# Optimization experiments

Measured on AMD Instinct MI355X. Metric: run time of the kernel, lower is better.

The kernel has to match this reference:

```python
import jax, jax.numpy as jnp
import numpy as np

N, E, EMB, H, HD, T, NG = 2048, 65536, 256, 8, 32, 24, 8


def _linear_params(key, din, dout):
    k1, k2 = jax.random.split(key)
    s = 1.0 / np.sqrt(din)
    W = jax.random.uniform(k1, (din, dout), minval=-s, maxval=s, dtype=jnp.float32)
    b = jax.random.uniform(k2, (dout,), minval=-s, maxval=s, dtype=jnp.float32)
    return W, b


def setup_inputs() -> dict:
    key = jax.random.key(0)
    ks = jax.random.split(key, 16)
    x = jax.random.normal(ks[0], (N, EMB), dtype=jnp.float32)
    edge_index = jax.random.randint(ks[1], (2, E), 0, N, dtype=jnp.int64)
    edge_attr = jax.random.normal(ks[2], (E, 4), dtype=jnp.float32)
    batch = jnp.sort(jax.random.randint(ks[3], (N,), 0, NG, dtype=jnp.int64))
    time_index = jax.random.randint(ks[4], (N,), 0, T, dtype=jnp.int64)
    temporal_embeddings = jax.random.normal(ks[5], (T, EMB), dtype=jnp.float32)
    Wq, bq = _linear_params(ks[6], EMB, EMB)
    Wk, bk = _linear_params(ks[7], EMB, EMB)
    Wv, bv = _linear_params(ks[8], EMB, EMB)
    Wo, bo = _linear_params(ks[9], EMB, EMB)
    We, be = _linear_params(ks[10], 4, H)
    Wtq, btq = _linear_params(ks[11], EMB, EMB)
    Wtk, btk = _linear_params(ks[12], EMB, EMB)
    Wtv, btv = _linear_params(ks[13], EMB, EMB)
    return dict(x=x, edge_index=edge_index, edge_attr=edge_attr, batch=batch,
                time_index=time_index, temporal_embeddings=temporal_embeddings,
                Wq=Wq, bq=bq, Wk=Wk, bk=bk, Wv=Wv, bv=bv, Wo=Wo, bo=bo,
                We=We, be=be, Wtq=Wtq, btq=btq, Wtk=Wtk, btk=btk, Wtv=Wtv, btv=btv)


def _heads(X, n):
    # [n, EMB] -> [H, n, HD]
    return X.reshape(n, H, HD).transpose(1, 0, 2)


def reference(x, edge_index, edge_attr, batch, time_index, temporal_embeddings,
              Wq, bq, Wk, bk, Wv, bv, Wo, bo, We, be, Wtq, btq, Wtk, btk, Wtv, btv):
    n = x.shape[0]
    scale = HD ** -0.5

    Qh = _heads(x @ Wq + bq, n)
    Kh = _heads(x @ Wk + bk, n)
    Vh = _heads(x @ Wv + bv, n)
    scores = jnp.einsum('hnd,hmd->hnm', Qh, Kh) * scale  # [H, n, n]

    # edge bias: vectorized scatter-add of per-edge per-head biases into [H, n, n]
    src, dst = edge_index[0], edge_index[1]
    valid = (src >= 0) & (src < n) & (dst >= 0) & (dst < n)
    eb = edge_attr @ We + be                              # [E, H]
    eb = jnp.where(valid[:, None], eb, 0.0)
    srcc = jnp.clip(src, 0, n - 1)
    dstc = jnp.clip(dst, 0, n - 1)
    scores = scores.at[:, srcc, dstc].add(eb.T)

    # batch mask: nodes may only attend within their own graph
    same_graph = batch[:, None] == batch[None, :]          # [n, n]
    scores = jnp.where(same_graph[None, :, :], scores, -jnp.inf)

    attn = jax.nn.softmax(scores, axis=-1)
    spatial_out = jnp.einsum('hnm,hmd->hnd', attn, Vh)     # [H, n, HD]

    # temporal attention on gathered temporal embeddings
    ti = jnp.clip(time_index, 0, temporal_embeddings.shape[0] - 1)
    emb = temporal_embeddings[ti]                          # [n, EMB]
    TQ = _heads(emb @ Wtq + btq, n)
    TK = _heads(emb @ Wtk + btk, n)
    TV = _heads(emb @ Wtv + btv, n)
    t_scores = jnp.einsum('hnd,hmd->hnm', TQ, TK) * scale
    t_scores = jnp.where(same_graph[None, :, :], t_scores, -jnp.inf)
    t_attn = jax.nn.softmax(t_scores, axis=-1)
    temporal_out = jnp.einsum('hnm,hmd->hnd', t_attn, TV)

    combined = (spatial_out + temporal_out).transpose(1, 0, 2).reshape(n, EMB)
    return combined @ Wo + bo
```

## Files before the change

### kernel.cpp

```cpp
#include <hip/hip_runtime.h>
#include <cstdint>
#include <cstddef>

#define EMB 256
#define NH 8
#define HD 32
#define NG 8
#define TMAX 24

#define LMAX 384
#define LB 384
#define TPB 6
#define VRU 200
#define FM 8.0f

typedef short s16x8 __attribute__((ext_vector_type(8)));
typedef float f32x4 __attribute__((ext_vector_type(4)));

__device__ __forceinline__ unsigned short f2b(float f) {
    unsigned u = __float_as_uint(f);
    return (unsigned short)((u + 0x7FFFu + ((u >> 16) & 1u)) >> 16);
}
__device__ __forceinline__ float b2f(unsigned short h) {
    return __uint_as_float((unsigned)h << 16);
}
__device__ __forceinline__ unsigned long long pack4(unsigned short a, unsigned short b,
                                                    unsigned short c, unsigned short d) {
    return (unsigned long long)a | ((unsigned long long)b << 16) |
           ((unsigned long long)c << 32) | ((unsigned long long)d << 48);
}

__device__ __forceinline__ size_t afrag_idx(int row, int k) {
    return ((size_t)((row >> 4) * 8 + (k >> 5)) << 9) +
           ((((k >> 3) & 3) * 16 + (row & 15)) << 3) + (k & 7);
}

struct PrepArgs {
    float4* Bias4; int bias4;
    const float* x; unsigned short* xh; unsigned short* xl;
    const float* temb; const int* ti; unsigned short* eh; unsigned short* el;
    const float* W[7]; unsigned short* whb; unsigned short* wlb;
    const int* batch; int* gstart; int n;
    int zb, cvtb;
};

__global__ __launch_bounds__(256) void k_prep(PrepArgs pa) {
    __shared__ float tile[32][33];
    int b = blockIdx.x;
    const int t = threadIdx.x;

    if (b < pa.zb) {
        int i = b * 256 + t;
        if (i < pa.bias4) pa.Bias4[i] = make_float4(0.f, 0.f, 0.f, 0.f);
        return;
    }
    b -= pa.zb;
    if (b < pa.cvtb) {
        int i = b * 256 + t;
        if (i < pa.n * (EMB / 4)) {
            int row = i >> 6, k4 = (i & 63) * 4;
            float4 v = ((const float4*)pa.x)[i];
            unsigned short h0 = f2b(v.x), h1 = f2b(v.y), h2 = f2b(v.z), h3 = f2b(v.w);
            size_t o = afrag_idx(row, k4) >> 2;
            ((unsigned long long*)pa.xh)[o] = pack4(h0, h1, h2, h3);
            ((unsigned long long*)pa.xl)[o] = pack4(f2b(v.x - b2f(h0)), f2b(v.y - b2f(h1)),
                                                    f2b(v.z - b2f(h2)), f2b(v.w - b2f(h3)));
        }
        return;
    }
    b -= pa.cvtb;
    if (b < pa.cvtb) {
        int idx = b * 256 + t;
        if (idx < pa.n * (EMB / 4)) {
            int row = idx >> 6, k4 = (idx & 63) * 4;
            int tt = pa.ti[row];
            tt = tt < 0 ? 0 : (tt > TMAX - 1 ? TMAX - 1 : tt);
            float4 v = ((const float4*)pa.temb)[tt * (EMB / 4) + (idx & 63)];
            unsigned short h0 = f2b(v.x), h1 = f2b(v.y), h2 = f2b(v.z), h3 = f2b(v.w);
            size_t o = afrag_idx(row, k4) >> 2;
            ((unsigned long long*)pa.eh)[o] = pack4(h0, h1, h2, h3);
            ((unsigned long long*)pa.el)[o] = pack4(f2b(v.x - b2f(h0)), f2b(v.y - b2f(h1)),
                                                    f2b(v.z - b2f(h2)), f2b(v.w - b2f(h3)));
        }
        return;
    }
    b -= pa.cvtb;
    if (b < 448) {
        const int z = b >> 6, rem = b & 63;
        const int k0 = (rem >> 3) << 5, n0 = (rem & 7) << 5;
        const float* W = pa.W[z];
        unsigned short* Wh = pa.whb + (size_t)z * 65536;
        unsigned short* Wl = pa.wlb + (size_t)z * 65536;
        {
            int rr = t >> 3, c4 = (t & 7) * 4;
            float4 v = *(const float4*)(W + (size_t)(k0 + rr) * 256 + n0 + c4);
            tile[rr][c4 + 0] = v.x; tile[rr][c4 + 1] = v.y;
            tile[rr][c4 + 2] = v.z; tile[rr][c4 + 3] = v.w;
        }
        __syncthreads();
        {
            int nn = n0 + (t >> 3), k4 = (t & 7) * 4;
            float v0 = tile[k4 + 0][t >> 3], v1 = tile[k4 + 1][t >> 3];
            float v2 = tile[k4 + 2][t >> 3], v3 = tile[k4 + 3][t >> 3];
            unsigned short h0 = f2b(v0), h1 = f2b(v1), h2 = f2b(v2), h3 = f2b(v3);
            size_t o = afrag_idx(nn, k0 + k4) >> 2;
            ((unsigned long long*)Wh)[o] = pack4(h0, h1, h2, h3);
            ((unsigned long long*)Wl)[o] = pack4(f2b(v0 - b2f(h0)), f2b(v1 - b2f(h1)),
                                                 f2b(v2 - b2f(h2)), f2b(v3 - b2f(h3)));
        }
        return;
    }
    if (t <= NG) {
        int lo = 0, hi = pa.n;
        while (lo < hi) {
            int mid = (lo + hi) >> 1;
            if (pa.batch[mid] < t) lo = mid + 1; else hi = mid;
        }
        pa.gstart[t] = lo;
    }
}

struct GB {
    const unsigned short* Ah[6];
    const unsigned short* Al[6];
    const float* bias[6];
    unsigned short* Chi[6];
    unsigned short* Clo[6];
    float cscale[6];
};

__global__ __launch_bounds__(256) void k_gemm_split(GB gb,
        const unsigned short* __restrict__ whb, const unsigned short* __restrict__ wlb, int M,
        const int* __restrict__ ei, const float* __restrict__ eattr,
        const float* __restrict__ We, const float* __restrict__ be,
        const int* __restrict__ batch, const int* __restrict__ gstart,
        float* __restrict__ Bias, int E) {
    const int z = blockIdx.z;
    const int t = threadIdx.x;

    if (z == 6) {
        const int stride = gridDim.x * gridDim.y * 256;
        for (int e = (blockIdx.y * gridDim.x + blockIdx.x) * 256 + t; e < E; e += stride) {
            int src = ei[e], dst = ei[E + e];
            if (src < 0 || src >= M || dst < 0 || dst >= M) continue;
            int bs = batch[src];
            if (bs != batch[dst]) continue;
            float4 a = *(const float4*)(eattr + (size_t)e * 4);
            int col = dst - gstart[bs];
#pragma unroll
            for (int h = 0; h < NH; h++) {
                float v = a.x * We[0 * NH + h] + a.y * We[1 * NH + h] +
                          a.z * We[2 * NH + h] + a.w * We[3 * NH + h] + be[h];
                atomicAdd(Bias + ((size_t)h * M + src) * LB + col, v);
            }
        }
        return;
    }

    const unsigned short* Ah = gb.Ah[z];
    const unsigned short* Al = gb.Al[z];
    const unsigned short* Wh = whb + (size_t)z * 65536;
    const unsigned short* Wl = wlb + (size_t)z * 65536;
    const float* bias = gb.bias[z];
    unsigned short* Chi = gb.Chi[z];
    unsigned short* Clo = gb.Clo[z];
    const float cs = gb.cscale[z];
    const bool fs = (Clo != nullptr);

    const int lane = t & 63, wv = t >> 6, lr = lane & 15, lq = lane >> 4;
    const int bm = blockIdx.x * 64 + (wv >> 1) * 32;
    const int bn = blockIdx.y * 64 + (wv & 1) * 32;
    const int mg0 = bm >> 4, ng0 = bn >> 4;

    f32x4 acc[2][2] = {};
#pragma unroll
    for (int kc = 0; kc < 8; kc++) {
        s16x8 ah[2], al[2], bh[2], bl[2];
#pragma unroll
        for (int mi = 0; mi < 2; mi++) {
            size_t o = ((size_t)((mg0 + mi) * 8 + kc) << 9) + lane * 8;
            ah[mi] = *(const s16x8*)(Ah + o);
            if (fs) al[mi] = *(const s16x8*)(Al + o);
        }
#pragma unroll
        for (int ni = 0; ni < 2; ni++) {
            size_t o = ((size_t)((ng0 + ni) * 8 + kc) << 9) + lane * 8;
            bh[ni] = *(const s16x8*)(Wh + o);
            bl[ni] = *(const s16x8*)(Wl + o);
        }
#pragma unroll
        for (int mi = 0; mi < 2; mi++)
#pragma unroll
            for (int ni = 0; ni < 2; ni++) {
                if (fs)
                    acc[mi][ni] = __builtin_amdgcn_mfma_f32_16x16x32_bf16(al[mi], bh[ni], acc[mi][ni], 0, 0, 0);
                acc[mi][ni] = __builtin_amdgcn_mfma_f32_16x16x32_bf16(ah[mi], bl[ni], acc[mi][ni], 0, 0, 0);
                acc[mi][ni] = __builtin_amdgcn_mfma_f32_16x16x32_bf16(ah[mi], bh[ni], acc[mi][ni], 0, 0, 0);
            }
    }
#pragma unroll
    for (int ni = 0; ni < 2; ni++) {
        const int col = bn + ni * 16 + lr;
        const int hh = col >> 5, dd = col & 31;
        float bv = bias[col];
#pragma unroll
        for (int mi = 0; mi < 2; mi++) {
#pragma unroll
            for (int r = 0; r < 4; r++) {
                int crow = bm + mi * 16 + 4 * lq + r;
                if (crow < M) {
                    float val = (acc[mi][ni][r] + bv) * cs;
                    unsigned short h = f2b(val);
                    size_t o = ((size_t)hh * M + crow) * HD + dd;
                    Chi[o] = h;
                    if (fs) Clo[o] = f2b(val - b2f(h));
                }
            }
        }
    }
}

__global__ __launch_bounds__(256) void k_attn5(
    const unsigned short* __restrict__ Qh, const unsigned short* __restrict__ Ql,
    const unsigned short* __restrict__ K, const unsigned short* __restrict__ V,
    const unsigned short* __restrict__ TQh, const unsigned short* __restrict__ TQl,
    const unsigned short* __restrict__ TK, const unsigned short* __restrict__ TV,
    const int* __restrict__ gstart, const float* __restrict__ Bias,
    float* __restrict__ comb, int n) {

    const int g  = blockIdx.x / TPB;
    const int tp = blockIdx.x % TPB;
    const int h  = blockIdx.y;
    const int gs = gstart[g], ge = gstart[g + 1];
    const int L  = ge - gs;
    const int q0b = tp * 64;
    if (q0b >= L) return;
    const int NC = (L + 31) >> 5;

    __shared__ __align__(16) unsigned int Vt[32 * VRU];
    __shared__ __align__(16) unsigned short Pb[4][16][40];

    const int t = threadIdx.x;
    const int wv = t >> 6, lane = t & 63;
    const int lr = lane & 15, lq = lane >> 4;
    const size_t hb = (size_t)h * n;

    const int q0w = q0b + wv * 16;
    int gq = gs + q0w + lr;
    if (gq > ge - 1) gq = ge - 1;

    float os0[4] = {0.f, 0.f, 0.f, 0.f};
    float os1[4] = {0.f, 0.f, 0.f, 0.f};

    for (int tz = 0; tz < 2; tz++) {
        const unsigned short* Qph = tz ? TQh : Qh;
        const unsigned short* Qpl = tz ? TQl : Ql;
        const unsigned short* Kp  = tz ? TK  : K;
        const unsigned short* Vp  = tz ? TV  : V;
        const bool hasb = (tz == 0);

        if (tz) __syncthreads();

        {
            const int d0 = (t & 7) * 4;
            for (int jp = t >> 3; jp < NC * 16; jp += 32) {
                int j0 = jp * 2;
                unsigned short a0 = 0, a1 = 0, a2 = 0, a3 = 0, b0 = 0, b1 = 0, b2 = 0, b3 = 0;
                if (j0 < L) {
                    const unsigned short* vp = Vp + (hb + gs + j0) * HD + d0;
                    a0 = vp[0]; a1 = vp[1]; a2 = vp[2]; a3 = vp[3];
                }
                if (j0 + 1 < L) {
                    const unsigned short* vp = Vp + (hb + gs + j0 + 1) * HD + d0;
                    b0 = vp[0]; b1 = vp[1]; b2 = vp[2]; b3 = vp[3];
                }
                Vt[(d0 + 0) * VRU + jp] = (unsigned)a0 | ((unsigned)b0 << 16);
                Vt[(d0 + 1) * VRU + jp] = (unsigned)a1 | ((unsigned)b1 << 16);
                Vt[(d0 + 2) * VRU + jp] = (unsigned)a2 | ((unsigned)b2 << 16);
                Vt[(d0 + 3) * VRU + jp] = (unsigned)a3 | ((unsigned)b3 << 16);
            }
        }

        s16x8 qfh = *(const s16x8*)(Qph + (hb + gq) * HD + lq * 8);
        s16x8 qfl = *(const s16x8*)(Qpl + (hb + gq) * HD + lq * 8);
        __syncthreads();

        const float* br0 = Bias; const float* br1 = Bias;
        const float* br2 = Bias; const float* br3 = Bias;
        if (hasb) {
            int r0 = gs + q0w + 4 * lq;
            int a0 = r0 + 0 < n ? r0 + 0 : n - 1;
            int a1 = r0 + 1 < n ? r0 + 1 : n - 1;
            int a2 = r0 + 2 < n ? r0 + 2 : n - 1;
            int a3 = r0 + 3 < n ? r0 + 3 : n - 1;
            br0 = Bias + (hb + a0) * LB;
            br1 = Bias + (hb + a1) * LB;
            br2 = Bias + (hb + a2) * LB;
            br3 = Bias + (hb + a3) * LB;
        }

        auto loadK = [&](int c, int half) -> s16x8 {
            int key = (2 * c + half) * 16 + lr;
            int krow = (key < L) ? (gs + key) : (ge - 1);
            return *(const s16x8*)(Kp + (hb + krow) * HD + lq * 8);
        };

        f32x4 acc0 = {0.f, 0.f, 0.f, 0.f};
        f32x4 acc1 = {0.f, 0.f, 0.f, 0.f};
        float ps0 = 0.f, ps1 = 0.f, ps2 = 0.f, ps3 = 0.f;

        s16x8 kfa = loadK(0, 0), kfb = loadK(0, 1);
        for (int c = 0; c < NC; c++) {
            const int cn = (c + 1 < NC) ? c + 1 : c;
            s16x8 nka = loadK(cn, 0), nkb = loadK(cn, 1);

            float p[2][4];
#pragma unroll
            for (int half = 0; half < 2; half++) {
                const int key = (2 * c + half) * 16 + lr;
                s16x8 kf = half ? kfb : kfa;
                f32x4 d = {0.f, 0.f, 0.f, 0.f};
                d = __builtin_amdgcn_mfma_f32_16x16x32_bf16(qfl, kf, d, 0, 0, 0);
                d = __builtin_amdgcn_mfma_f32_16x16x32_bf16(qfh, kf, d, 0, 0, 0);
                float s0 = d[0], s1 = d[1], s2 = d[2], s3 = d[3];
                if (hasb) {
                    s0 += br0[key]; s1 += br1[key]; s2 += br2[key]; s3 += br3[key];
                }
                const bool ok = key < L;
                s0 = ok ? s0 : -3.0e38f;
                s1 = ok ? s1 : -3.0e38f;
                s2 = ok ? s2 : -3.0e38f;
                s3 = ok ? s3 : -3.0e38f;
                p[half][0] = __expf(s0 - FM);
                p[half][1] = __expf(s1 - FM);
                p[half][2] = __expf(s2 - FM);
                p[half][3] = __expf(s3 - FM);
            }
            ps0 += p[0][0] + p[1][0];
            ps1 += p[0][1] + p[1][1];
            ps2 += p[0][2] + p[1][2];
            ps3 += p[0][3] + p[1][3];
#pragma unroll
            for (int half = 0; half < 2; half++) {
#pragma unroll
                for (int r = 0; r < 4; r++)
                    Pb[wv][4 * lq + r][half * 16 + lr] = f2b(p[half][r]);
            }
            s16x8 pf  = *(const s16x8*)&Pb[wv][lr][8 * lq];
            s16x8 vf0 = *(const s16x8*)&Vt[(size_t)lr * VRU + c * 16 + lq * 4];
            s16x8 vf1 = *(const s16x8*)&Vt[(size_t)(16 + lr) * VRU + c * 16 + lq * 4];
            acc0 = __builtin_amdgcn_mfma_f32_16x16x32_bf16(pf, vf0, acc0, 0, 0, 0);
            acc1 = __builtin_amdgcn_mfma_f32_16x16x32_bf16(pf, vf1, acc1, 0, 0, 0);
            kfa = nka; kfb = nkb;
        }

#pragma unroll
        for (int m = 1; m < 16; m <<= 1) {
            ps0 += __shfl_xor(ps0, m, 16);
            ps1 += __shfl_xor(ps1, m, 16);
            ps2 += __shfl_xor(ps2, m, 16);
            ps3 += __shfl_xor(ps3, m, 16);
        }
        float iv0 = 1.0f / ps0, iv1 = 1.0f / ps1, iv2 = 1.0f / ps2, iv3 = 1.0f / ps3;
        os0[0] += acc0[0] * iv0; os1[0] += acc1[0] * iv0;
        os0[1] += acc0[1] * iv1; os1[1] += acc1[1] * iv1;
        os0[2] += acc0[2] * iv2; os1[2] += acc1[2] * iv2;
        os0[3] += acc0[3] * iv3; os1[3] += acc1[3] * iv3;
    }

    const int qb = q0w + 4 * lq;
#pragma unroll
    for (int r = 0; r < 4; r++) {
        if (qb + r < L) {
            float* op = comb + (hb + gs + qb + r) * HD + lr;
            op[0]  = os0[r];
            op[16] = os1[r];
        }
    }
}

__global__ __launch_bounds__(256) void k_gemm_out(const float* __restrict__ A,
        const unsigned short* __restrict__ Wh, const unsigned short* __restrict__ Wl,
        const float* __restrict__ bias, float* __restrict__ C, int M) {
    const int t = threadIdx.x;
    const int lane = t & 63, wv = t >> 6, lr = lane & 15, lq = lane >> 4;
    const int bm = blockIdx.x * 64 + (wv >> 1) * 32;
    const int bn = blockIdx.y * 64 + (wv & 1) * 32;
    const int ng0 = bn >> 4;

    int ra[2], cb[2];
#pragma unroll
    for (int mi = 0; mi < 2; mi++) {
        int r = bm + mi * 16 + lr;
        ra[mi] = r < M ? r : M - 1;
    }
#pragma unroll
    for (int ni = 0; ni < 2; ni++) cb[ni] = bn + ni * 16 + lr;

    f32x4 acc[2][2] = {};
#pragma unroll
    for (int kc = 0; kc < 8; kc++) {
        s16x8 ah[2], al[2], bh[2], bl[2];
#pragma unroll
        for (int mi = 0; mi < 2; mi++) {
            size_t off = ((size_t)kc * M + ra[mi]) * HD + lq * 8;
            float4 a = *(const float4*)(A + off);
            float4 b = *(const float4*)(A + off + 4);
            float vv[8] = {a.x, a.y, a.z, a.w, b.x, b.y, b.z, b.w};
#pragma unroll
            for (int j = 0; j < 8; j++) {
                unsigned short hh = f2b(vv[j]);
                ah[mi][j] = (short)hh;
                al[mi][j] = (short)f2b(vv[j] - b2f(hh));
            }
        }
#pragma unroll
        for (int ni = 0; ni < 2; ni++) {
            size_t o = ((size_t)((ng0 + ni) * 8 + kc) << 9) + lane * 8;
            bh[ni] = *(const s16x8*)(Wh + o);
            bl[ni] = *(const s16x8*)(Wl + o);
        }
#pragma unroll
        for (int mi = 0; mi < 2; mi++)
#pragma unroll
            for (int ni = 0; ni < 2; ni++) {
                acc[mi][ni] = __builtin_amdgcn_mfma_f32_16x16x32_bf16(al[mi], bh[ni], acc[mi][ni], 0, 0, 0);
                acc[mi][ni] = __builtin_amdgcn_mfma_f32_16x16x32_bf16(ah[mi], bl[ni], acc[mi][ni], 0, 0, 0);
                acc[mi][ni] = __builtin_amdgcn_mfma_f32_16x16x32_bf16(ah[mi], bh[ni], acc[mi][ni], 0, 0, 0);
            }
    }
#pragma unroll
    for (int ni = 0; ni < 2; ni++) {
        float bv = bias[cb[ni]];
#pragma unroll
        for (int mi = 0; mi < 2; mi++) {
#pragma unroll
            for (int r = 0; r < 4; r++) {
                int crow = bm + mi * 16 + 4 * lq + r;
                if (crow < M)
                    C[(size_t)crow * 256 + cb[ni]] = acc[mi][ni][r] + bv;
            }
        }
    }
}

extern "C" void kernel_launch(void* const* d_in, const int* in_sizes, int n_in,
                              void* d_out, int out_size, void* d_ws, size_t ws_size,
                              hipStream_t stream) {
    const float* x     = (const float*)d_in[0];
    const int*   ei    = (const int*)d_in[1];
    const float* eattr = (const float*)d_in[2];
    const int*   batch = (const int*)d_in[3];
    const int*   ti    = (const int*)d_in[4];
    const float* temb  = (const float*)d_in[5];
    const float* Wq = (const float*)d_in[6],  *bq = (const float*)d_in[7];
    const float* Wk = (const float*)d_in[8],  *bk = (const float*)d_in[9];
    const float* Wv = (const float*)d_in[10], *bv = (const float*)d_in[11];
    const float* Wo = (const float*)d_in[12], *bo = (const float*)d_in[13];
    const float* We = (const float*)d_in[14], *be = (const float*)d_in[15];
    const float* Wtq = (const float*)d_in[16], *btq = (const float*)d_in[17];
    const float* Wtk = (const float*)d_in[18], *btk = (const float*)d_in[19];
    const float* Wtv = (const float*)d_in[20], *btv = (const float*)d_in[21];

    const int n = in_sizes[0] / EMB;
    const int E = in_sizes[2] / 4;
    float* out = (float*)d_out;

    char* w = (char*)d_ws;
    auto alloc = [&](size_t bytes) -> void* {
        void* p = (void*)w;
        w += (bytes + 255) & ~(size_t)255;
        return p;
    };
    const size_t nb = (size_t)n * EMB * 2;
    unsigned short* xh   = (unsigned short*)alloc(nb);
    unsigned short* xl   = (unsigned short*)alloc(nb);
    unsigned short* eh   = (unsigned short*)alloc(nb);
    unsigned short* el   = (unsigned short*)alloc(nb);
    unsigned short* whb  = (unsigned short*)alloc((size_t)7 * 65536 * 2);
    unsigned short* wlb  = (unsigned short*)alloc((size_t)7 * 65536 * 2);
    unsigned short* Qhb  = (unsigned short*)alloc(nb);
    unsigned short* Qlb  = (unsigned short*)alloc(nb);
    unsigned short* Kb   = (unsigned short*)alloc(nb);
    unsigned short* Vb   = (unsigned short*)alloc(nb);
    unsigned short* TQhb = (unsigned short*)alloc(nb);
    unsigned short* TQlb = (unsigned short*)alloc(nb);
    unsigned short* TKb  = (unsigned short*)alloc(nb);
    unsigned short* TVb  = (unsigned short*)alloc(nb);
    float* Bias  = (float*)alloc((size_t)NH * n * LB * 4);
    float* comb  = (float*)alloc((size_t)n * EMB * 4);
    int* gstart  = (int*)alloc((NG + 1) * 4);

    PrepArgs pa;
    pa.Bias4 = (float4*)Bias;
    pa.bias4 = NH * n * LB / 4;
    pa.x = x; pa.xh = xh; pa.xl = xl;
    pa.temb = temb; pa.ti = ti; pa.eh = eh; pa.el = el;
    pa.W[0] = Wq; pa.W[1] = Wk; pa.W[2] = Wv;
    pa.W[3] = Wtq; pa.W[4] = Wtk; pa.W[5] = Wtv; pa.W[6] = Wo;
    pa.whb = whb; pa.wlb = wlb;
    pa.batch = batch; pa.gstart = gstart; pa.n = n;
    pa.zb = (pa.bias4 + 255) / 256;
    pa.cvtb = (n * (EMB / 4) + 255) / 256;
    const int prep_blocks = pa.zb + 2 * pa.cvtb + 448 + 1;
    k_prep<<<dim3(prep_blocks), dim3(256), 0, stream>>>(pa);

    const float scale = 0.17677669529663687f;
    GB gb;
    gb.Ah[0] = xh; gb.Al[0] = xl; gb.bias[0] = bq;  gb.Chi[0] = Qhb;  gb.Clo[0] = Qlb;  gb.cscale[0] = scale;
    gb.Ah[1] = xh; gb.Al[1] = xl; gb.bias[1] = bk;  gb.Chi[1] = Kb;   gb.Clo[1] = nullptr; gb.cscale[1] = 1.f;
    gb.Ah[2] = xh; gb.Al[2] = xl; gb.bias[2] = bv;  gb.Chi[2] = Vb;   gb.Clo[2] = nullptr; gb.cscale[2] = 1.f;
    gb.Ah[3] = eh; gb.Al[3] = el; gb.bias[3] = btq; gb.Chi[3] = TQhb; gb.Clo[3] = TQlb; gb.cscale[3] = scale;
    gb.Ah[4] = eh; gb.Al[4] = el; gb.bias[4] = btk; gb.Chi[4] = TKb;  gb.Clo[4] = nullptr; gb.cscale[4] = 1.f;
    gb.Ah[5] = eh; gb.Al[5] = el; gb.bias[5] = btv; gb.Chi[5] = TVb;  gb.Clo[5] = nullptr; gb.cscale[5] = 1.f;
    k_gemm_split<<<dim3((n + 63) / 64, EMB / 64, 7), dim3(256), 0, stream>>>(
        gb, whb, wlb, n, ei, eattr, We, be, batch, gstart, Bias, E);

    k_attn5<<<dim3(NG * TPB, NH), dim3(256), 0, stream>>>(Qhb, Qlb, Kb, Vb,
                                                          TQhb, TQlb, TKb, TVb,
                                                          gstart, Bias, comb, n);
    k_gemm_out<<<dim3((n + 63) / 64, EMB / 64), dim3(256), 0, stream>>>(
        comb, whb + (size_t)6 * 65536, wlb + (size_t)6 * 65536, bo, out, n);
}
```

Before: 61.01 us.

## Split attention key range across two blocks and merge partials in output GEMM

The attention kernel now splits each graph's key chunks across a new grid dimension of two, writing unnormalized partial P·V accumulators and row sums to scratch buffers. The output GEMM reads both partials for spatial and temporal attention, sums them, and normalizes before converting to bf16 hi/lo. Since a fixed max offset is used, no max rescaling is needed for the merge. This doubles the attention grid to improve occupancy on the many-CU device, in exchange for extra scratch writes and reads and more work in the output GEMM's load path.

```diff
diff --git a/kernel.cpp b/kernel.cpp
--- a/kernel.cpp
+++ b/kernel.cpp
@@ -13,6 +13,7 @@
 #define TPB 6
 #define VRU 200
 #define FM 8.0f
+#define KS 2
 
 typedef short s16x8 __attribute__((ext_vector_type(8)));
 typedef float f32x4 __attribute__((ext_vector_type(4)));
@@ -220,22 +221,26 @@
     }
 }
 
-__global__ __launch_bounds__(256) void k_attn5(
+__global__ __launch_bounds__(256) void k_attn6(
     const unsigned short* __restrict__ Qh, const unsigned short* __restrict__ Ql,
     const unsigned short* __restrict__ K, const unsigned short* __restrict__ V,
     const unsigned short* __restrict__ TQh, const unsigned short* __restrict__ TQl,
     const unsigned short* __restrict__ TK, const unsigned short* __restrict__ TV,
     const int* __restrict__ gstart, const float* __restrict__ Bias,
-    float* __restrict__ comb, int n) {
+    float* __restrict__ U, float* __restrict__ PS, int n) {
 
     const int g  = blockIdx.x / TPB;
     const int tp = blockIdx.x % TPB;
     const int h  = blockIdx.y;
+    const int ks = blockIdx.z;
     const int gs = gstart[g], ge = gstart[g + 1];
     const int L  = ge - gs;
     const int q0b = tp * 64;
     if (q0b >= L) return;
-    const int NC = (L + 31) >> 5;
+    const int NC  = (L + 31) >> 5;
+    const int NCH = (NC + KS - 1) / KS;
+    const int c0  = ks * NCH;
+    const int c1  = (c0 + NCH < NC) ? (c0 + NCH) : NC;
 
     __shared__ __align__(16) unsigned int Vt[32 * VRU];
     __shared__ __align__(16) unsigned short Pb[4][16][40];
@@ -248,9 +253,7 @@
     const int q0w = q0b + wv * 16;
     int gq = gs + q0w + lr;
     if (gq > ge - 1) gq = ge - 1;
-
-    float os0[4] = {0.f, 0.f, 0.f, 0.f};
-    float os1[4] = {0.f, 0.f, 0.f, 0.f};
+    const int qb = q0w + 4 * lq;
 
     for (int tz = 0; tz < 2; tz++) {
         const unsigned short* Qph = tz ? TQh : Qh;
@@ -262,9 +265,10 @@
         if (tz) __syncthreads();
 
         {
+            const int NPAIR = (c1 - c0) * 16;
             const int d0 = (t & 7) * 4;
-            for (int jp = t >> 3; jp < NC * 16; jp += 32) {
-                int j0 = jp * 2;
+            for (int jp = t >> 3; jp < NPAIR; jp += 32) {
+                int j0 = c0 * 32 + jp * 2;
                 unsigned short a0 = 0, a1 = 0, a2 = 0, a3 = 0, b0 = 0, b1 = 0, b2 = 0, b3 = 0;
                 if (j0 < L) {
                     const unsigned short* vp = Vp + (hb + gs + j0) * HD + d0;
@@ -309,49 +313,51 @@
         f32x4 acc1 = {0.f, 0.f, 0.f, 0.f};
         float ps0 = 0.f, ps1 = 0.f, ps2 = 0.f, ps3 = 0.f;
 
-        s16x8 kfa = loadK(0, 0), kfb = loadK(0, 1);
-        for (int c = 0; c < NC; c++) {
-            const int cn = (c + 1 < NC) ? c + 1 : c;
-            s16x8 nka = loadK(cn, 0), nkb = loadK(cn, 1);
-
-            float p[2][4];
-#pragma unroll
-            for (int half = 0; half < 2; half++) {
-                const int key = (2 * c + half) * 16 + lr;
-                s16x8 kf = half ? kfb : kfa;
-                f32x4 d = {0.f, 0.f, 0.f, 0.f};
-                d = __builtin_amdgcn_mfma_f32_16x16x32_bf16(qfl, kf, d, 0, 0, 0);
-                d = __builtin_amdgcn_mfma_f32_16x16x32_bf16(qfh, kf, d, 0, 0, 0);
-                float s0 = d[0], s1 = d[1], s2 = d[2], s3 = d[3];
-                if (hasb) {
-                    s0 += br0[key]; s1 += br1[key]; s2 += br2[key]; s3 += br3[key];
+        if (c0 < c1) {
+            s16x8 kfa = loadK(c0, 0), kfb = loadK(c0, 1);
+            for (int c = c0; c < c1; c++) {
+                const int cn = (c + 1 < c1) ? c + 1 : c;
+                s16x8 nka = loadK(cn, 0), nkb = loadK(cn, 1);
+
+                float p[2][4];
+#pragma unroll
+                for (int half = 0; half < 2; half++) {
+                    const int key = (2 * c + half) * 16 + lr;
+                    s16x8 kf = half ? kfb : kfa;
+                    f32x4 d = {0.f, 0.f, 0.f, 0.f};
+                    d = __builtin_amdgcn_mfma_f32_16x16x32_bf16(qfl, kf, d, 0, 0, 0);
+                    d = __builtin_amdgcn_mfma_f32_16x16x32_bf16(qfh, kf, d, 0, 0, 0);
+                    float s0 = d[0], s1 = d[1], s2 = d[2], s3 = d[3];
+                    if (hasb) {
+                        s0 += br0[key]; s1 += br1[key]; s2 += br2[key]; s3 += br3[key];
+                    }
+                    const bool ok = key < L;
+                    s0 = ok ? s0 : -3.0e38f;
+                    s1 = ok ? s1 : -3.0e38f;
+                    s2 = ok ? s2 : -3.0e38f;
+                    s3 = ok ? s3 : -3.0e38f;
+                    p[half][0] = __expf(s0 - FM);
+                    p[half][1] = __expf(s1 - FM);
+                    p[half][2] = __expf(s2 - FM);
+                    p[half][3] = __expf(s3 - FM);
                 }
-                const bool ok = key < L;
-                s0 = ok ? s0 : -3.0e38f;
-                s1 = ok ? s1 : -3.0e38f;
-                s2 = ok ? s2 : -3.0e38f;
-                s3 = ok ? s3 : -3.0e38f;
-                p[half][0] = __expf(s0 - FM);
-                p[half][1] = __expf(s1 - FM);
-                p[half][2] = __expf(s2 - FM);
-                p[half][3] = __expf(s3 - FM);
-            }
-            ps0 += p[0][0] + p[1][0];
-            ps1 += p[0][1] + p[1][1];
-            ps2 += p[0][2] + p[1][2];
-            ps3 += p[0][3] + p[1][3];
-#pragma unroll
-            for (int half = 0; half < 2; half++) {
-#pragma unroll
-                for (int r = 0; r < 4; r++)
-                    Pb[wv][4 * lq + r][half * 16 + lr] = f2b(p[half][r]);
-            }
-            s16x8 pf  = *(const s16x8*)&Pb[wv][lr][8 * lq];
-            s16x8 vf0 = *(const s16x8*)&Vt[(size_t)lr * VRU + c * 16 + lq * 4];
-            s16x8 vf1 = *(const s16x8*)&Vt[(size_t)(16 + lr) * VRU + c * 16 + lq * 4];
-            acc0 = __builtin_amdgcn_mfma_f32_16x16x32_bf16(pf, vf0, acc0, 0, 0, 0);
-            acc1 = __builtin_amdgcn_mfma_f32_16x16x32_bf16(pf, vf1, acc1, 0, 0, 0);
-            kfa = nka; kfb = nkb;
+                ps0 += p[0][0] + p[1][0];
+                ps1 += p[0][1] + p[1][1];
+                ps2 += p[0][2] + p[1][2];
+                ps3 += p[0][3] + p[1][3];
+#pragma unroll
+                for (int half = 0; half < 2; half++) {
+#pragma unroll
+                    for (int r = 0; r < 4; r++)
+                        Pb[wv][4 * lq + r][half * 16 + lr] = f2b(p[half][r]);
+                }
+                s16x8 pf  = *(const s16x8*)&Pb[wv][lr][8 * lq];
+                s16x8 vf0 = *(const s16x8*)&Vt[(size_t)lr * VRU + (c - c0) * 16 + lq * 4];
+                s16x8 vf1 = *(const s16x8*)&Vt[(size_t)(16 + lr) * VRU + (c - c0) * 16 + lq * 4];
+                acc0 = __builtin_amdgcn_mfma_f32_16x16x32_bf16(pf, vf0, acc0, 0, 0, 0);
+                acc1 = __builtin_amdgcn_mfma_f32_16x16x32_bf16(pf, vf1, acc1, 0, 0, 0);
+                kfa = nka; kfb = nkb;
+            }
         }
 
 #pragma unroll
@@ -361,25 +367,28 @@
             ps2 += __shfl_xor(ps2, m, 16);
             ps3 += __shfl_xor(ps3, m, 16);
         }
-        float iv0 = 1.0f / ps0, iv1 = 1.0f / ps1, iv2 = 1.0f / ps2, iv3 = 1.0f / ps3;
-        os0[0] += acc0[0] * iv0; os1[0] += acc1[0] * iv0;
-        os0[1] += acc0[1] * iv1; os1[1] += acc1[1] * iv1;
-        os0[2] += acc0[2] * iv2; os1[2] += acc1[2] * iv2;
-        os0[3] += acc0[3] * iv3; os1[3] += acc1[3] * iv3;
-    }
-
-    const int qb = q0w + 4 * lq;
-#pragma unroll
-    for (int r = 0; r < 4; r++) {
-        if (qb + r < L) {
-            float* op = comb + (hb + gs + qb + r) * HD + lr;
-            op[0]  = os0[r];
-            op[16] = os1[r];
-        }
-    }
-}
-
-__global__ __launch_bounds__(256) void k_gemm_out(const float* __restrict__ A,
+
+        float* Up  = U  + ((size_t)(ks * 2 + tz) * NH + h) * ((size_t)n * HD);
+        float* PSp = PS + ((size_t)(ks * 2 + tz) * NH + h) * (size_t)n;
+#pragma unroll
+        for (int r = 0; r < 4; r++) {
+            if (qb + r < L) {
+                float* op = Up + (size_t)(gs + qb + r) * HD + lr;
+                op[0]  = acc0[r];
+                op[16] = acc1[r];
+            }
+        }
+        if (lr == 0) {
+            if (qb + 0 < L) PSp[gs + qb + 0] = ps0;
+            if (qb + 1 < L) PSp[gs + qb + 1] = ps1;
+            if (qb + 2 < L) PSp[gs + qb + 2] = ps2;
+            if (qb + 3 < L) PSp[gs + qb + 3] = ps3;
+        }
+    }
+}
+
+__global__ __launch_bounds__(256) void k_gemm_out(const float* __restrict__ U,
+        const float* __restrict__ PS,
         const unsigned short* __restrict__ Wh, const unsigned short* __restrict__ Wl,
         const float* __restrict__ bias, float* __restrict__ C, int M) {
     const int t = threadIdx.x;
@@ -388,6 +397,9 @@
     const int bn = blockIdx.y * 64 + (wv & 1) * 32;
     const int ng0 = bn >> 4;
 
+    const size_t PLU = (size_t)NH * M * HD;
+    const size_t PLS = (size_t)NH * M;
+
     int ra[2], cb[2];
 #pragma unroll
     for (int mi = 0; mi < 2; mi++) {
@@ -403,10 +415,28 @@
         s16x8 ah[2], al[2], bh[2], bl[2];
 #pragma unroll
         for (int mi = 0; mi < 2; mi++) {
-            size_t off = ((size_t)kc * M + ra[mi]) * HD + lq * 8;
-            float4 a = *(const float4*)(A + off);
-            float4 b = *(const float4*)(A + off + 4);
-            float vv[8] = {a.x, a.y, a.z, a.w, b.x, b.y, b.z, b.w};
+            const size_t off = ((size_t)kc * M + ra[mi]) * HD + lq * 8;
+            const size_t ips = (size_t)kc * M + ra[mi];
+            float rs = 1.0f / (PS[ips] + PS[2 * PLS + ips]);
+            float rt = 1.0f / (PS[PLS + ips] + PS[3 * PLS + ips]);
+            float4 s0a = *(const float4*)(U + off);
+            float4 s0b = *(const float4*)(U + off + 4);
+            float4 s1a = *(const float4*)(U + 2 * PLU + off);
+            float4 s1b = *(const float4*)(U + 2 * PLU + off + 4);
+            float4 t0a = *(const float4*)(U + PLU + off);
+            float4 t0b = *(const float4*)(U + PLU + off + 4);
+            float4 t1a = *(const float4*)(U + 3 * PLU + off);
+            float4 t1b = *(const float4*)(U + 3 * PLU + off + 4);
+            float vv[8] = {
+                (s0a.x + s1a.x) * rs + (t0a.x + t1a.x) * rt,
+                (s0a.y + s1a.y) * rs + (t0a.y + t1a.y) * rt,
+                (s0a.z + s1a.z) * rs + (t0a.z + t1a.z) * rt,
+                (s0a.w + s1a.w) * rs + (t0a.w + t1a.w) * rt,
+                (s0b.x + s1b.x) * rs + (t0b.x + t1b.x) * rt,
+                (s0b.y + s1b.y) * rs + (t0b.y + t1b.y) * rt,
+                (s0b.z + s1b.z) * rs + (t0b.z + t1b.z) * rt,
+                (s0b.w + s1b.w) * rs + (t0b.w + t1b.w) * rt,
+            };
 #pragma unroll
             for (int j = 0; j < 8; j++) {
                 unsigned short hh = f2b(vv[j]);
@@ -488,7 +518,8 @@
     unsigned short* TKb  = (unsigned short*)alloc(nb);
     unsigned short* TVb  = (unsigned short*)alloc(nb);
     float* Bias  = (float*)alloc((size_t)NH * n * LB * 4);
-    float* comb  = (float*)alloc((size_t)n * EMB * 4);
+    float* U     = (float*)alloc((size_t)2 * KS * NH * n * HD * 4);
+    float* PSb   = (float*)alloc((size_t)2 * KS * NH * n * 4);
     int* gstart  = (int*)alloc((NG + 1) * 4);
 
     PrepArgs pa;
@@ -516,9 +547,9 @@
     k_gemm_split<<<dim3((n + 63) / 64, EMB / 64, 7), dim3(256), 0, stream>>>(
         gb, whb, wlb, n, ei, eattr, We, be, batch, gstart, Bias, E);
 
-    k_attn5<<<dim3(NG * TPB, NH), dim3(256), 0, stream>>>(Qhb, Qlb, Kb, Vb,
-                                                          TQhb, TQlb, TKb, TVb,
-                                                          gstart, Bias, comb, n);
+    k_attn6<<<dim3(NG * TPB, NH, KS), dim3(256), 0, stream>>>(Qhb, Qlb, Kb, Vb,
+                                                              TQhb, TQlb, TKb, TVb,
+                                                              gstart, Bias, U, PSb, n);
     k_gemm_out<<<dim3((n + 63) / 64, EMB / 64), dim3(256), 0, stream>>>(
-        comb, whb + (size_t)6 * 65536, wlb + (size_t)6 * 65536, bo, out, n);
-}
+        U, PSb, whb + (size_t)6 * 65536, wlb + (size_t)6 * 65536, bo, out, n);
+}
```

Result: slower. 65.59 us (+7.5%).

## Emit bf16 hi/lo fragments from attention and shrink output GEMM tiles

Applied to the files above, without the earlier changes.

The attention kernel now splits its output into bf16 high/low pairs and writes them straight into MFMA A-fragment layout (afrag_idx), so the float combined buffer goes away. The output GEMM loads those pre-split fragments directly, with no per-element conversion. It also moves to one-wave blocks with 16x32 tiles, which gives many more blocks for better occupancy. The cost is scattered 2-byte stores in the attention epilogue, and the GEMM drops its bounds checks by assuming n is a multiple of 16.

```diff
diff --git a/kernel.cpp b/kernel.cpp
--- a/kernel.cpp
+++ b/kernel.cpp
@@ -226,7 +226,7 @@
     const unsigned short* __restrict__ TQh, const unsigned short* __restrict__ TQl,
     const unsigned short* __restrict__ TK, const unsigned short* __restrict__ TV,
     const int* __restrict__ gstart, const float* __restrict__ Bias,
-    float* __restrict__ comb, int n) {
+    unsigned short* __restrict__ ch, unsigned short* __restrict__ cl, int n) {
 
     const int g  = blockIdx.x / TPB;
     const int tp = blockIdx.x % TPB;
@@ -372,74 +372,54 @@
 #pragma unroll
     for (int r = 0; r < 4; r++) {
         if (qb + r < L) {
-            float* op = comb + (hb + gs + qb + r) * HD + lr;
-            op[0]  = os0[r];
-            op[16] = os1[r];
-        }
-    }
-}
-
-__global__ __launch_bounds__(256) void k_gemm_out(const float* __restrict__ A,
+            const int grow = gs + qb + r;
+            float v0 = os0[r], v1 = os1[r];
+            unsigned short h0 = f2b(v0);
+            unsigned short l0 = f2b(v0 - b2f(h0));
+            unsigned short h1 = f2b(v1);
+            unsigned short l1 = f2b(v1 - b2f(h1));
+            size_t o0 = afrag_idx(grow, h * HD + lr);
+            size_t o1 = afrag_idx(grow, h * HD + 16 + lr);
+            ch[o0] = h0; cl[o0] = l0;
+            ch[o1] = h1; cl[o1] = l1;
+        }
+    }
+}
+
+__global__ __launch_bounds__(64) void k_gemm_out(const unsigned short* __restrict__ Ah,
+        const unsigned short* __restrict__ Al,
         const unsigned short* __restrict__ Wh, const unsigned short* __restrict__ Wl,
         const float* __restrict__ bias, float* __restrict__ C, int M) {
-    const int t = threadIdx.x;
-    const int lane = t & 63, wv = t >> 6, lr = lane & 15, lq = lane >> 4;
-    const int bm = blockIdx.x * 64 + (wv >> 1) * 32;
-    const int bn = blockIdx.y * 64 + (wv & 1) * 32;
-    const int ng0 = bn >> 4;
-
-    int ra[2], cb[2];
-#pragma unroll
-    for (int mi = 0; mi < 2; mi++) {
-        int r = bm + mi * 16 + lr;
-        ra[mi] = r < M ? r : M - 1;
-    }
-#pragma unroll
-    for (int ni = 0; ni < 2; ni++) cb[ni] = bn + ni * 16 + lr;
-
-    f32x4 acc[2][2] = {};
+    const int lane = threadIdx.x;
+    const int lr = lane & 15, lq = lane >> 4;
+    const int bm = blockIdx.x * 16;
+    const int bn = blockIdx.y * 32;
+    const int mg = bm >> 4, ng0 = bn >> 4;
+
+    f32x4 acc[2] = {};
 #pragma unroll
     for (int kc = 0; kc < 8; kc++) {
-        s16x8 ah[2], al[2], bh[2], bl[2];
-#pragma unroll
-        for (int mi = 0; mi < 2; mi++) {
-            size_t off = ((size_t)kc * M + ra[mi]) * HD + lq * 8;
-            float4 a = *(const float4*)(A + off);
-            float4 b = *(const float4*)(A + off + 4);
-            float vv[8] = {a.x, a.y, a.z, a.w, b.x, b.y, b.z, b.w};
-#pragma unroll
-            for (int j = 0; j < 8; j++) {
-                unsigned short hh = f2b(vv[j]);
-                ah[mi][j] = (short)hh;
-                al[mi][j] = (short)f2b(vv[j] - b2f(hh));
-            }
-        }
+        size_t oa = ((size_t)(mg * 8 + kc) << 9) + lane * 8;
+        s16x8 ah = *(const s16x8*)(Ah + oa);
+        s16x8 al = *(const s16x8*)(Al + oa);
 #pragma unroll
         for (int ni = 0; ni < 2; ni++) {
-            size_t o = ((size_t)((ng0 + ni) * 8 + kc) << 9) + lane * 8;
-            bh[ni] = *(const s16x8*)(Wh + o);
-            bl[ni] = *(const s16x8*)(Wl + o);
-        }
-#pragma unroll
-        for (int mi = 0; mi < 2; mi++)
-#pragma unroll
-            for (int ni = 0; ni < 2; ni++) {
-                acc[mi][ni] = __builtin_amdgcn_mfma_f32_16x16x32_bf16(al[mi], bh[ni], acc[mi][ni], 0, 0, 0);
-                acc[mi][ni] = __builtin_amdgcn_mfma_f32_16x16x32_bf16(ah[mi], bl[ni], acc[mi][ni], 0, 0, 0);
-                acc[mi][ni] = __builtin_amdgcn_mfma_f32_16x16x32_bf16(ah[mi], bh[ni], acc[mi][ni], 0, 0, 0);
-            }
+            size_t ob = ((size_t)((ng0 + ni) * 8 + kc) << 9) + lane * 8;
+            s16x8 bh = *(const s16x8*)(Wh + ob);
+            s16x8 bl = *(const s16x8*)(Wl + ob);
+            acc[ni] = __builtin_amdgcn_mfma_f32_16x16x32_bf16(al, bh, acc[ni], 0, 0, 0);
+            acc[ni] = __builtin_amdgcn_mfma_f32_16x16x32_bf16(ah, bl, acc[ni], 0, 0, 0);
+            acc[ni] = __builtin_amdgcn_mfma_f32_16x16x32_bf16(ah, bh, acc[ni], 0, 0, 0);
+        }
     }
 #pragma unroll
     for (int ni = 0; ni < 2; ni++) {
-        float bv = bias[cb[ni]];
-#pragma unroll
-        for (int mi = 0; mi < 2; mi++) {
-#pragma unroll
-            for (int r = 0; r < 4; r++) {
-                int crow = bm + mi * 16 + 4 * lq + r;
-                if (crow < M)
-                    C[(size_t)crow * 256 + cb[ni]] = acc[mi][ni][r] + bv;
-            }
+        const int col = bn + ni * 16 + lr;
+        float bv = bias[col];
+#pragma unroll
+        for (int r = 0; r < 4; r++) {
+            const int crow = bm + 4 * lq + r;
+            C[(size_t)crow * 256 + col] = acc[ni][r] + bv;
         }
     }
 }
@@ -488,7 +468,8 @@
     unsigned short* TKb  = (unsigned short*)alloc(nb);
     unsigned short* TVb  = (unsigned short*)alloc(nb);
     float* Bias  = (float*)alloc((size_t)NH * n * LB * 4);
-    float* comb  = (float*)alloc((size_t)n * EMB * 4);
+    unsigned short* ch = (unsigned short*)alloc(nb);
+    unsigned short* cl = (unsigned short*)alloc(nb);
     int* gstart  = (int*)alloc((NG + 1) * 4);
 
     PrepArgs pa;
@@ -518,7 +499,7 @@
 
     k_attn5<<<dim3(NG * TPB, NH), dim3(256), 0, stream>>>(Qhb, Qlb, Kb, Vb,
                                                           TQhb, TQlb, TKb, TVb,
-                                                          gstart, Bias, comb, n);
-    k_gemm_out<<<dim3((n + 63) / 64, EMB / 64), dim3(256), 0, stream>>>(
-        comb, whb + (size_t)6 * 65536, wlb + (size_t)6 * 65536, bo, out, n);
-}
+                                                          gstart, Bias, ch, cl, n);
+    k_gemm_out<<<dim3(n / 16, EMB / 32), dim3(64), 0, stream>>>(
+        ch, cl, whb + (size_t)6 * 65536, wlb + (size_t)6 * 65536, bo, out, n);
+}
```

New measurement: 56.94 us. 6.7% less time.
